# Optimization experiments

Measured on AMD Instinct MI355X. Metric: run time of the kernel, lower is better.

## Reference

```python
import jax, jax.numpy as jnp
import numpy as np

B, H, N_OBS, N_DIR = 4096, 1024, 128, 64
MAX_ITER, LR_ITER, TOL = 10, 1e-3, 1e-3


def _norm(x):
    # row-wise L2 normalization, matching self.norm
    return x / (jnp.linalg.norm(x, axis=1, keepdims=True) + 1e-6)


def setup_inputs() -> dict:
    key = jax.random.key(0)
    ks = jax.random.split(key, 6)
    directions = jax.random.randint(ks[0], (B,), 0, N_DIR)
    obs = jax.random.randint(ks[1], (B,), 0, N_OBS)
    Wr = jax.random.normal(ks[2], (H, H), jnp.float32)
    Win = jax.random.normal(ks[3], (H, N_DIR), jnp.float32)
    Wout = jax.random.normal(ks[4], (N_OBS, H), jnp.float32) * 2.0
    prev_states = _norm(jax.random.normal(ks[5], (B, H), jnp.float32))
    return dict(directions=directions, obs=obs, Wr=Wr, Win=Win,
                Wout=Wout, prev_states=prev_states)


def reference(directions, obs, Wr, Win, Wout, prev_states):
    dtype = Wr.dtype
    dir_e = jax.nn.one_hot(directions, N_DIR, dtype=dtype)  # [B, n_dir]
    obs_e = jax.nn.one_hot(obs, N_OBS, dtype=dtype)         # [B, n_obs]

    drive = jnp.einsum('hd,bd->bh', Win, dir_e)
    cur = _norm(jax.nn.relu(jnp.einsum('hk,bk->bh', Wr, prev_states) + drive))
    prev = prev_states
    done = jnp.array(False)

    def step(carry, _):
        prev, cur, done = carry
        # while condition: |mean(prev - cur)| > tol (checked before each update)
        cond = jnp.abs(jnp.mean(prev - cur)) > TOL
        active = jnp.logical_and(jnp.logical_not(done), cond)

        logits = jnp.einsum('oh,bh->bo', Wout, cur)          # [B, n_obs]
        f = jax.nn.softmax(logits, axis=1)
        eps_p = obs_e - f
        # softmax-Jacobian vector product: J @ v = f * (v - <f, v>)
        Jv = f * (eps_p - jnp.sum(f * eps_p, axis=1, keepdims=True))
        eps_g = cur - jax.nn.relu(jnp.einsum('hk,bk->bh', Wr, prev) + drive)
        new_cur = _norm(cur + LR_ITER * (-eps_g + jnp.einsum('oh,bo->bh', Wout, Jv)))

        prev_n = jnp.where(active, cur, prev)
        cur_n = jnp.where(active, new_cur, cur)
        done_n = jnp.logical_or(done, jnp.logical_not(cond))
        return (prev_n, cur_n, done_n), None

    (prev, cur, done), _ = jax.lax.scan(step, (prev, cur, done), None, length=MAX_ITER)
    next_obs_preds = jax.nn.softmax(jnp.einsum('oh,bh->bo', Wout, cur), axis=1)
    return next_obs_preds, cur
```

## Files before the change

kernel.cpp:

```cpp
#include <hip/hip_runtime.h>
#include <cstdint>
#include <cstddef>

#define B_    4096
#define H_    1024
#define NOBS  128
#define NDIR  64
#define MAXIT 10
#define LRI   1e-3f
#define TOLC  1e-3
#define KS_   8

typedef __bf16 bf16x8 __attribute__((ext_vector_type(8)));
typedef float  f32x4  __attribute__((ext_vector_type(4)));

__device__ __forceinline__ ushort f2bf(float x) {
    uint32_t u = __float_as_uint(x);
    u += 0x7FFFu + ((u >> 16) & 1u);
    return (ushort)(u >> 16);
}
__device__ __forceinline__ float bf2f(ushort h) {
    return __uint_as_float(((uint32_t)h) << 16);
}

template<int ROWS>
__device__ __forceinline__ void stage_tile(ushort* dst, const ushort* src,
                                           size_t rowbase, int ld, int k0,
                                           int tid, int wid)
{
    constexpr int ITERS = ROWS * 4 / 256;
#pragma unroll
    for (int cc = 0; cc < ITERS; ++cc) {
        const int c = cc * 256 + tid;
        const int r = c >> 2, s = c & 3;
        const int ks = ((s ^ ((r >> 1) & 3)) << 3);
        const ushort* g = src + (rowbase + r) * (size_t)ld + k0 + ks;
        __builtin_amdgcn_global_load_lds(
            (const __attribute__((address_space(1))) void*)g,
            (__attribute__((address_space(3))) void*)(dst + (cc * 256 + wid * 64) * 8),
            16, 0, 0);
    }
}

template<int EPI, int BN>
__global__ __launch_bounds__(256)
void gemm_pipe_k(const ushort* __restrict__ Ahi, const ushort* __restrict__ Alo, int lda,
                 const ushort* __restrict__ Bhi, const ushort* __restrict__ Blo, int ldb,
                 float* __restrict__ O,
                 const int* __restrict__ dirs, const float* __restrict__ Win,
                 const float* __restrict__ Cin,
                 const int* gate)
{
    if (gate && *gate == 0) return;

    constexpr int NFR = BN / 32;
    constexpr int NST = (EPI == 0) ? H_ / 32
                      : (EPI == 1) ? (H_ / KS_) / 32
                                   : NOBS / 32;

    __shared__ ushort sA[2][2][128 * 32];
    __shared__ ushort sB[2][2][BN * 32];

    const int tid = threadIdx.x, lane = tid & 63, wid = tid >> 6;
    const size_t m0  = (size_t)blockIdx.y * 128;
    const size_t bn0 = (EPI == 1) ? 0 : (size_t)blockIdx.x * BN;
    const int kbase  = (EPI == 1) ? blockIdx.x * (H_ / KS_) : 0;
    const int wr = wid >> 1, wc = wid & 1;

    f32x4 acc[4][NFR];
#pragma unroll
    for (int i = 0; i < 4; ++i)
#pragma unroll
        for (int j = 0; j < NFR; ++j) acc[i][j] = (f32x4){0.f, 0.f, 0.f, 0.f};

    const int rsel = lane & 15;
    const int kb   = lane >> 4;

    stage_tile<128>(sA[0][0], Ahi, m0, lda, kbase, tid, wid);
    stage_tile<128>(sA[0][1], Alo, m0, lda, kbase, tid, wid);
    stage_tile<BN >(sB[0][0], Bhi, bn0, ldb, kbase, tid, wid);
    stage_tile<BN >(sB[0][1], Blo, bn0, ldb, kbase, tid, wid);
    __syncthreads();

#pragma unroll 2
    for (int t = 0; t < NST; ++t) {
        const int cur = t & 1;
        if (t + 1 < NST) {
            const int k0 = kbase + (t + 1) * 32;
            stage_tile<128>(sA[cur ^ 1][0], Ahi, m0, lda, k0, tid, wid);
            stage_tile<128>(sA[cur ^ 1][1], Alo, m0, lda, k0, tid, wid);
            stage_tile<BN >(sB[cur ^ 1][0], Bhi, bn0, ldb, k0, tid, wid);
            stage_tile<BN >(sB[cur ^ 1][1], Blo, bn0, ldb, k0, tid, wid);
        }

        bf16x8 ah[4], al[4], bh[NFR], bl[NFR];
#pragma unroll
        for (int f = 0; f < 4; ++f) {
            const int arow = wr * 64 + f * 16 + rsel;
            const int aoff = arow * 32 + ((kb ^ ((arow >> 1) & 3)) << 3);
            ah[f] = *(const bf16x8*)&sA[cur][0][aoff];
            al[f] = *(const bf16x8*)&sA[cur][1][aoff];
        }
#pragma unroll
        for (int f = 0; f < NFR; ++f) {
            const int brow = wc * (BN / 2) + f * 16 + rsel;
            const int boff = brow * 32 + ((kb ^ ((brow >> 1) & 3)) << 3);
            bh[f] = *(const bf16x8*)&sB[cur][0][boff];
            bl[f] = *(const bf16x8*)&sB[cur][1][boff];
        }

#pragma unroll
        for (int i = 0; i < 4; ++i)
#pragma unroll
            for (int j = 0; j < NFR; ++j) {
                acc[i][j] = __builtin_amdgcn_mfma_f32_16x16x32_bf16(ah[i], bh[j], acc[i][j], 0, 0, 0);
                acc[i][j] = __builtin_amdgcn_mfma_f32_16x16x32_bf16(ah[i], bl[j], acc[i][j], 0, 0, 0);
                acc[i][j] = __builtin_amdgcn_mfma_f32_16x16x32_bf16(al[i], bh[j], acc[i][j], 0, 0, 0);
            }
        __syncthreads();
    }

    float* pout = (EPI == 1) ? O + (size_t)blockIdx.x * B_ * NOBS : O;
#pragma unroll
    for (int i = 0; i < 4; ++i) {
#pragma unroll
        for (int r = 0; r < 4; ++r) {
            const size_t row = m0 + wr * 64 + i * 16 + (lane >> 4) * 4 + r;
            int dd = 0;
            if (EPI == 0) dd = dirs[row];
#pragma unroll
            for (int j = 0; j < NFR; ++j) {
                const size_t col = bn0 + wc * (BN / 2) + j * 16 + (lane & 15);
                if (EPI == 0) {
                    const float v = acc[i][j][r] + Win[col * NDIR + dd];
                    pout[row * H_ + col] = fmaxf(v, 0.f);
                } else if (EPI == 1) {
                    pout[row * NOBS + col] = acc[i][j][r];
                } else {
                    const size_t idx = row * H_ + col;
                    const float c = Cin[idx], rv = pout[idx];
                    pout[idx] = c + LRI * ((rv - c) + acc[i][j][r]);
                }
            }
        }
    }
}

template<int MODE>
__global__ __launch_bounds__(256)
void softjv_k(const float* __restrict__ part, const int* __restrict__ obs,
              ushort* __restrict__ Jhi, ushort* __restrict__ Jlo,
              float* __restrict__ probs, const int* gate)
{
    if (MODE == 0 && gate && *gate == 0) return;
    const int wid = threadIdx.x >> 6, lane = threadIdx.x & 63;
    const int b = blockIdx.x * 4 + wid;
    float x0 = 0.f, x1 = 0.f;
#pragma unroll
    for (int kb = 0; kb < KS_; ++kb) {
        const float* p = part + ((size_t)kb * B_ + b) * NOBS;
        x0 += p[lane]; x1 += p[lane + 64];
    }
    float mx = fmaxf(x0, x1);
#pragma unroll
    for (int off = 32; off > 0; off >>= 1) mx = fmaxf(mx, __shfl_xor(mx, off, 64));
    const float e0 = expf(x0 - mx), e1 = expf(x1 - mx);
    float s = e0 + e1;
#pragma unroll
    for (int off = 32; off > 0; off >>= 1) s += __shfl_xor(s, off, 64);
    const float f0 = e0 / s, f1 = e1 / s;
    if (MODE == 1) {
        probs[(size_t)b * NOBS + lane]      = f0;
        probs[(size_t)b * NOBS + lane + 64] = f1;
        return;
    }
    const int o = obs[b];
    const float ep0 = ((lane == o) ? 1.f : 0.f) - f0;
    const float ep1 = ((lane + 64 == o) ? 1.f : 0.f) - f1;
    float d = f0 * ep0 + f1 * ep1;
#pragma unroll
    for (int off = 32; off > 0; off >>= 1) d += __shfl_xor(d, off, 64);
    const float j0 = f0 * (ep0 - d), j1 = f1 * (ep1 - d);
    const ushort h0 = f2bf(j0), h1 = f2bf(j1);
    Jhi[(size_t)b * NOBS + lane]      = h0;
    Jlo[(size_t)b * NOBS + lane]      = f2bf(j0 - bf2f(h0));
    Jhi[(size_t)b * NOBS + lane + 64] = h1;
    Jlo[(size_t)b * NOBS + lane + 64] = f2bf(j1 - bf2f(h1));
}

template<bool ADV>
__global__ __launch_bounds__(256)
void normadv_k(const float* __restrict__ T, float* __restrict__ C,
               ushort* __restrict__ Chi, ushort* __restrict__ Clo,
               ushort* __restrict__ Phi, ushort* __restrict__ Plo,
               const float* __restrict__ oldsum, float* __restrict__ rowsum,
               double* __restrict__ rowpart, const int* gate)
{
    if (gate && *gate == 0) return;
    const int b = blockIdx.x, tid = threadIdx.x;
    const size_t ro = (size_t)b * H_;

    if (ADV) {
        ((ushort4*)(Phi + ro))[tid] = ((const ushort4*)(Chi + ro))[tid];
        ((ushort4*)(Plo + ro))[tid] = ((const ushort4*)(Clo + ro))[tid];
    }

    const float4 v = ((const float4*)(T + ro))[tid];
    float ss = v.x * v.x + v.y * v.y + v.z * v.z + v.w * v.w;
    float sm = v.x + v.y + v.z + v.w;
#pragma unroll
    for (int off = 32; off > 0; off >>= 1) {
        ss += __shfl_down(ss, off, 64);
        sm += __shfl_down(sm, off, 64);
    }
    __shared__ float w1[4], w2[4];
    const int lane = tid & 63, wid = tid >> 6;
    if (lane == 0) { w1[wid] = ss; w2[wid] = sm; }
    __syncthreads();
    const float tot = w1[0] + w1[1] + w1[2] + w1[3];
    const float smt = w2[0] + w2[1] + w2[2] + w2[3];
    const float d = sqrtf(tot) + 1e-6f;

    float4 o;
    o.x = v.x / d; o.y = v.y / d; o.z = v.z / d; o.w = v.w / d;
    ((float4*)(C + ro))[tid] = o;
    ushort4 h, l;
    h.x = f2bf(o.x); l.x = f2bf(o.x - bf2f(h.x));
    h.y = f2bf(o.y); l.y = f2bf(o.y - bf2f(h.y));
    h.z = f2bf(o.z); l.z = f2bf(o.z - bf2f(h.z));
    h.w = f2bf(o.w); l.w = f2bf(o.w - bf2f(h.w));
    ((ushort4*)(Chi + ro))[tid] = h;
    ((ushort4*)(Clo + ro))[tid] = l;

    if (tid == 0) {
        const float news = smt / d;
        rowpart[b] = (double)oldsum[b] - (double)news;
        rowsum[b]  = news;
    }
}

__global__ __launch_bounds__(256)
void cond_fin_k(const double* __restrict__ rowpart, int* active, int* done)
{
    if (*done) { if (threadIdx.x == 0) *active = 0; return; }
    __shared__ double wsum[4];
    double s = 0.0;
    for (int i = threadIdx.x; i < B_; i += 256) s += rowpart[i];
#pragma unroll
    for (int off = 32; off > 0; off >>= 1) s += __shfl_down(s, off, 64);
    const int lane = threadIdx.x & 63, wid = threadIdx.x >> 6;
    if (lane == 0) wsum[wid] = s;
    __syncthreads();
    if (threadIdx.x == 0) {
        const double mean = (wsum[0] + wsum[1] + wsum[2] + wsum[3]) / (double)((size_t)B_ * H_);
        const int c = (fabs(mean) > TOLC) ? 1 : 0;
        *active = c;
        if (!c) *done = 1;
    }
}

__global__ __launch_bounds__(256)
void split_k(const float* __restrict__ x, ushort* __restrict__ hi,
             ushort* __restrict__ lo)
{
    const size_t i = (size_t)blockIdx.x * 256 + threadIdx.x;
    const float4 v = ((const float4*)x)[i];
    ushort4 h, l;
    h.x = f2bf(v.x); l.x = f2bf(v.x - bf2f(h.x));
    h.y = f2bf(v.y); l.y = f2bf(v.y - bf2f(h.y));
    h.z = f2bf(v.z); l.z = f2bf(v.z - bf2f(h.z));
    h.w = f2bf(v.w); l.w = f2bf(v.w - bf2f(h.w));
    ((ushort4*)hi)[i] = h;
    ((ushort4*)lo)[i] = l;
}

__global__ __launch_bounds__(256)
void prev0_prep_k(const float* __restrict__ prev0, ushort* __restrict__ Phi,
                  ushort* __restrict__ Plo, float* __restrict__ prevsum0)
{
    const int b = blockIdx.x, tid = threadIdx.x;
    const size_t ro = (size_t)b * H_;
    const float4 v = ((const float4*)(prev0 + ro))[tid];
    ushort4 h, l;
    h.x = f2bf(v.x); l.x = f2bf(v.x - bf2f(h.x));
    h.y = f2bf(v.y); l.y = f2bf(v.y - bf2f(h.y));
    h.z = f2bf(v.z); l.z = f2bf(v.z - bf2f(h.z));
    h.w = f2bf(v.w); l.w = f2bf(v.w - bf2f(h.w));
    ((ushort4*)(Phi + ro))[tid] = h;
    ((ushort4*)(Plo + ro))[tid] = l;
    float sm = v.x + v.y + v.z + v.w;
#pragma unroll
    for (int off = 32; off > 0; off >>= 1) sm += __shfl_down(sm, off, 64);
    __shared__ float w2[4];
    const int lane = tid & 63, wid = tid >> 6;
    if (lane == 0) w2[wid] = sm;
    __syncthreads();
    if (tid == 0) prevsum0[b] = w2[0] + w2[1] + w2[2] + w2[3];
}

__global__ __launch_bounds__(256)
void prep_wout_k(const float* __restrict__ Wout, ushort* __restrict__ Whi,
                 ushort* __restrict__ Wlo, ushort* __restrict__ WThi,
                 ushort* __restrict__ WTlo)
{
    const int idx = blockIdx.x * 256 + threadIdx.x;
    const float w = Wout[idx];
    const ushort h = f2bf(w), l = f2bf(w - bf2f(h));
    Whi[idx] = h; Wlo[idx] = l;
    const int o = idx >> 10, hh = idx & 1023;
    WThi[(size_t)hh * NOBS + o] = h;
    WTlo[(size_t)hh * NOBS + o] = l;
}

__global__ __launch_bounds__(256)
void copy_k(const float* __restrict__ src, float* __restrict__ dst)
{
    const size_t i = (size_t)blockIdx.x * 256 + threadIdx.x;
    ((float4*)dst)[i] = ((const float4*)src)[i];
}

__global__ void flags_init_k(int* flags) { flags[0] = 0; flags[1] = 0; }

extern "C" void kernel_launch(void* const* d_in, const int* in_sizes, int n_in,
                              void* d_out, int out_size, void* d_ws, size_t ws_size,
                              hipStream_t stream)
{
    const int*   dirs  = (const int*)d_in[0];
    const int*   obs   = (const int*)d_in[1];
    const float* Wr    = (const float*)d_in[2];
    const float* Win   = (const float*)d_in[3];
    const float* Wout  = (const float*)d_in[4];
    const float* prev0 = (const float*)d_in[5];
    float* out = (float*)d_out;

    const size_t SZ = (size_t)B_ * H_;
    float*  C    = (float*)d_ws;
    float*  T    = C + SZ;
    float*  part = T + SZ;
    ushort* Chi  = (ushort*)(part + (size_t)KS_ * B_ * NOBS);
    ushort* Clo  = Chi + SZ;
    ushort* Phi  = Clo + SZ;
    ushort* Plo  = Phi + SZ;
    ushort* Wrhi = Plo + SZ;
    ushort* Wrlo = Wrhi + (size_t)H_ * H_;
    ushort* Whi  = Wrlo + (size_t)H_ * H_;
    ushort* Wlo  = Whi + (size_t)NOBS * H_;
    ushort* WThi = Wlo + (size_t)NOBS * H_;
    ushort* WTlo = WThi + (size_t)H_ * NOBS;
    ushort* Jhi  = WTlo + (size_t)H_ * NOBS;
    ushort* Jlo  = Jhi + (size_t)B_ * NOBS;
    double* rowpart = (double*)(Jlo + (size_t)B_ * NOBS);
    float* prevsum0 = (float*)(rowpart + B_);
    float* rowsumC  = prevsum0 + B_;
    int* flags  = (int*)(rowsumC + B_);
    int* done   = flags;
    int* active = flags + 1;

    const dim3 blk(256);
    const dim3 gBig(H_ / 64, B_ / 128);
    const dim3 gLog(KS_, B_ / 128);

    flags_init_k<<<1, 1, 0, stream>>>(flags);
    split_k<<<(H_ * H_ / 4) / 256, blk, 0, stream>>>(Wr, Wrhi, Wrlo);
    prev0_prep_k<<<B_, blk, 0, stream>>>(prev0, Phi, Plo, prevsum0);
    prep_wout_k<<<(NOBS * H_) / 256, blk, 0, stream>>>(Wout, Whi, Wlo, WThi, WTlo);

    gemm_pipe_k<0, 64><<<gBig, blk, 0, stream>>>(
        Phi, Plo, H_, Wrhi, Wrlo, H_, T, dirs, Win, nullptr, nullptr);
    normadv_k<false><<<B_, blk, 0, stream>>>(
        T, C, Chi, Clo, nullptr, nullptr, prevsum0, rowsumC, rowpart, nullptr);

    for (int it = 0; it < MAXIT; ++it) {
        cond_fin_k<<<1, blk, 0, stream>>>(rowpart, active, done);

        if (it > 0)
            gemm_pipe_k<0, 64><<<gBig, blk, 0, stream>>>(
                Phi, Plo, H_, Wrhi, Wrlo, H_, T, dirs, Win, nullptr, active);
        gemm_pipe_k<1, 128><<<gLog, blk, 0, stream>>>(
            Chi, Clo, H_, Whi, Wlo, H_, part, nullptr, nullptr, nullptr, active);
        softjv_k<0><<<B_ / 4, blk, 0, stream>>>(part, obs, Jhi, Jlo, nullptr, active);
        gemm_pipe_k<2, 64><<<gBig, blk, 0, stream>>>(
            Jhi, Jlo, NOBS, WThi, WTlo, NOBS, T, nullptr, nullptr, C, active);
        normadv_k<true><<<B_, blk, 0, stream>>>(
            T, C, Chi, Clo, Phi, Plo, rowsumC, rowsumC, rowpart, active);
    }

    gemm_pipe_k<1, 128><<<gLog, blk, 0, stream>>>(
        Chi, Clo, H_, Whi, Wlo, H_, part, nullptr, nullptr, nullptr, nullptr);
    softjv_k<1><<<B_ / 4, blk, 0, stream>>>(part, obs, nullptr, nullptr, out, nullptr);
    copy_k<<<SZ / 4 / 256, blk, 0, stream>>>(C, out + (size_t)B_ * NOBS);
}
```

Measured before the change: 314.3 us.

## Add dedicated 128x128 Wr GEMM kernel with 32x32 MFMA and triple-buffered loads

Replaces the generic pipelined GEMM used for the dominant Wr @ prev product with a specialized kernel. It uses 128x128 output tiles, 32x32x16 bf16 MFMA instructions and a three-stage LDS ring with explicit vmcnt waits and barriers, so global loads run two tiles ahead. The generic kernel loses its Wr epilogue and fully unrolls its short K loops. The aim is more operand reuse per LDS read and better hiding of load latency. The cost is higher LDS use (96 KB per block), which lowers occupancy, and half as many blocks for this GEMM.

New measurement: 320.5 us. About the same (+2.0%).

```diff
diff --git a/kernel.cpp b/kernel.cpp
--- a/kernel.cpp
+++ b/kernel.cpp
@@ -13,6 +13,7 @@
 
 typedef __bf16 bf16x8 __attribute__((ext_vector_type(8)));
 typedef float  f32x4  __attribute__((ext_vector_type(4)));
+typedef float  f32x16 __attribute__((ext_vector_type(16)));
 
 __device__ __forceinline__ ushort f2bf(float x) {
     uint32_t u = __float_as_uint(x);
@@ -42,21 +43,128 @@
     }
 }
 
+__global__ __launch_bounds__(256)
+void wr_gemm_k(const ushort* __restrict__ Ahi, const ushort* __restrict__ Alo,
+               const ushort* __restrict__ Bhi, const ushort* __restrict__ Blo,
+               float* __restrict__ O,
+               const int* __restrict__ dirs, const float* __restrict__ Win,
+               const int* gate)
+{
+    if (gate && *gate == 0) return;
+
+    constexpr int NST = H_ / 32;
+    __shared__ ushort sA[3][2][128 * 32];
+    __shared__ ushort sB[3][2][128 * 32];
+
+    const int tid = threadIdx.x, lane = tid & 63, wid = tid >> 6;
+    const size_t m0 = (size_t)blockIdx.y * 128;
+    const size_t n0 = (size_t)blockIdx.x * 128;
+    const int wr = wid >> 1, wc = wid & 1;
+
+    f32x16 acc[2][2];
+#pragma unroll
+    for (int i = 0; i < 2; ++i)
+#pragma unroll
+        for (int j = 0; j < 2; ++j)
+#pragma unroll
+            for (int r = 0; r < 16; ++r) acc[i][j][r] = 0.f;
+
+    stage_tile<128>(sA[0][0], Ahi, m0, H_, 0, tid, wid);
+    stage_tile<128>(sA[0][1], Alo, m0, H_, 0, tid, wid);
+    stage_tile<128>(sB[0][0], Bhi, n0, H_, 0, tid, wid);
+    stage_tile<128>(sB[0][1], Blo, n0, H_, 0, tid, wid);
+    __builtin_amdgcn_sched_barrier(0);
+    stage_tile<128>(sA[1][0], Ahi, m0, H_, 32, tid, wid);
+    stage_tile<128>(sA[1][1], Alo, m0, H_, 32, tid, wid);
+    stage_tile<128>(sB[1][0], Bhi, n0, H_, 32, tid, wid);
+    stage_tile<128>(sB[1][1], Blo, n0, H_, 32, tid, wid);
+    __builtin_amdgcn_sched_barrier(0);
+
+    int cur = 0;
+#pragma unroll 1
+    for (int t = 0; t < NST; ++t) {
+        if (t + 1 < NST) asm volatile("s_waitcnt vmcnt(8)" ::: "memory");
+        else             asm volatile("s_waitcnt vmcnt(0)" ::: "memory");
+        __builtin_amdgcn_sched_barrier(0);
+        __builtin_amdgcn_s_barrier();
+        __builtin_amdgcn_sched_barrier(0);
+
+        if (t + 2 < NST) {
+            const int nbuf = (cur >= 1) ? cur - 1 : cur + 2;
+            const int k0 = (t + 2) * 32;
+            stage_tile<128>(sA[nbuf][0], Ahi, m0, H_, k0, tid, wid);
+            stage_tile<128>(sA[nbuf][1], Alo, m0, H_, k0, tid, wid);
+            stage_tile<128>(sB[nbuf][0], Bhi, n0, H_, k0, tid, wid);
+            stage_tile<128>(sB[nbuf][1], Blo, n0, H_, k0, tid, wid);
+        }
+        __builtin_amdgcn_sched_barrier(0);
+
+        const ushort* pAh = sA[cur][0];
+        const ushort* pAl = sA[cur][1];
+        const ushort* pBh = sB[cur][0];
+        const ushort* pBl = sB[cur][1];
+
+#pragma unroll
+        for (int s = 0; s < 2; ++s) {
+            bf16x8 ah[2], al[2], bh[2], bl[2];
+            const int e8 = s * 2 + (lane >> 5);
+#pragma unroll
+            for (int mb = 0; mb < 2; ++mb) {
+                const int row = wr * 64 + mb * 32 + (lane & 31);
+                const int off = row * 32 + ((e8 ^ ((row >> 1) & 3)) << 3);
+                ah[mb] = *(const bf16x8*)&pAh[off];
+                al[mb] = *(const bf16x8*)&pAl[off];
+            }
+#pragma unroll
+            for (int nb = 0; nb < 2; ++nb) {
+                const int row = wc * 64 + nb * 32 + (lane & 31);
+                const int off = row * 32 + ((e8 ^ ((row >> 1) & 3)) << 3);
+                bh[nb] = *(const bf16x8*)&pBh[off];
+                bl[nb] = *(const bf16x8*)&pBl[off];
+            }
+#pragma unroll
+            for (int mb = 0; mb < 2; ++mb)
+#pragma unroll
+                for (int nb = 0; nb < 2; ++nb) {
+                    acc[mb][nb] = __builtin_amdgcn_mfma_f32_32x32x16_bf16(ah[mb], bh[nb], acc[mb][nb], 0, 0, 0);
+                    acc[mb][nb] = __builtin_amdgcn_mfma_f32_32x32x16_bf16(ah[mb], bl[nb], acc[mb][nb], 0, 0, 0);
+                    acc[mb][nb] = __builtin_amdgcn_mfma_f32_32x32x16_bf16(al[mb], bh[nb], acc[mb][nb], 0, 0, 0);
+                }
+        }
+
+        __builtin_amdgcn_sched_barrier(0);
+        __builtin_amdgcn_s_barrier();
+        cur = (cur == 2) ? 0 : cur + 1;
+    }
+
+#pragma unroll
+    for (int mb = 0; mb < 2; ++mb)
+#pragma unroll
+        for (int reg = 0; reg < 16; ++reg) {
+            const size_t row = m0 + wr * 64 + mb * 32 +
+                               (reg & 3) + 8 * (reg >> 2) + 4 * (lane >> 5);
+            const int dd = dirs[row];
+#pragma unroll
+            for (int nb = 0; nb < 2; ++nb) {
+                const size_t col = n0 + wc * 64 + nb * 32 + (lane & 31);
+                const float v = acc[mb][nb][reg] + Win[col * NDIR + dd];
+                O[row * H_ + col] = fmaxf(v, 0.f);
+            }
+        }
+}
+
 template<int EPI, int BN>
 __global__ __launch_bounds__(256)
 void gemm_pipe_k(const ushort* __restrict__ Ahi, const ushort* __restrict__ Alo, int lda,
                  const ushort* __restrict__ Bhi, const ushort* __restrict__ Blo, int ldb,
                  float* __restrict__ O,
-                 const int* __restrict__ dirs, const float* __restrict__ Win,
                  const float* __restrict__ Cin,
                  const int* gate)
 {
     if (gate && *gate == 0) return;
 
     constexpr int NFR = BN / 32;
-    constexpr int NST = (EPI == 0) ? H_ / 32
-                      : (EPI == 1) ? (H_ / KS_) / 32
-                                   : NOBS / 32;
+    constexpr int NST = (EPI == 1) ? (H_ / KS_) / 32 : NOBS / 32;
 
     __shared__ ushort sA[2][2][128 * 32];
     __shared__ ushort sB[2][2][BN * 32];
@@ -82,7 +190,7 @@
     stage_tile<BN >(sB[0][1], Blo, bn0, ldb, kbase, tid, wid);
     __syncthreads();
 
-#pragma unroll 2
+#pragma unroll
     for (int t = 0; t < NST; ++t) {
         const int cur = t & 1;
         if (t + 1 < NST) {
@@ -126,15 +234,10 @@
 #pragma unroll
         for (int r = 0; r < 4; ++r) {
             const size_t row = m0 + wr * 64 + i * 16 + (lane >> 4) * 4 + r;
-            int dd = 0;
-            if (EPI == 0) dd = dirs[row];
 #pragma unroll
             for (int j = 0; j < NFR; ++j) {
                 const size_t col = bn0 + wc * (BN / 2) + j * 16 + (lane & 15);
-                if (EPI == 0) {
-                    const float v = acc[i][j][r] + Win[col * NDIR + dd];
-                    pout[row * H_ + col] = fmaxf(v, 0.f);
-                } else if (EPI == 1) {
+                if (EPI == 1) {
                     pout[row * NOBS + col] = acc[i][j][r];
                 } else {
                     const size_t idx = row * H_ + col;
@@ -357,7 +460,8 @@
     int* active = flags + 1;
 
     const dim3 blk(256);
-    const dim3 gBig(H_ / 64, B_ / 128);
+    const dim3 gBig(H_ / 128, B_ / 128);
+    const dim3 gUpd(H_ / 64, B_ / 128);
     const dim3 gLog(KS_, B_ / 128);
 
     flags_init_k<<<1, 1, 0, stream>>>(flags);
@@ -365,8 +469,7 @@
     prev0_prep_k<<<B_, blk, 0, stream>>>(prev0, Phi, Plo, prevsum0);
     prep_wout_k<<<(NOBS * H_) / 256, blk, 0, stream>>>(Wout, Whi, Wlo, WThi, WTlo);
 
-    gemm_pipe_k<0, 64><<<gBig, blk, 0, stream>>>(
-        Phi, Plo, H_, Wrhi, Wrlo, H_, T, dirs, Win, nullptr, nullptr);
+    wr_gemm_k<<<gBig, blk, 0, stream>>>(Phi, Plo, Wrhi, Wrlo, T, dirs, Win, nullptr);
     normadv_k<false><<<B_, blk, 0, stream>>>(
         T, C, Chi, Clo, nullptr, nullptr, prevsum0, rowsumC, rowpart, nullptr);
 
@@ -374,19 +477,18 @@
         cond_fin_k<<<1, blk, 0, stream>>>(rowpart, active, done);
 
         if (it > 0)
-            gemm_pipe_k<0, 64><<<gBig, blk, 0, stream>>>(
-                Phi, Plo, H_, Wrhi, Wrlo, H_, T, dirs, Win, nullptr, active);
+            wr_gemm_k<<<gBig, blk, 0, stream>>>(Phi, Plo, Wrhi, Wrlo, T, dirs, Win, active);
         gemm_pipe_k<1, 128><<<gLog, blk, 0, stream>>>(
-            Chi, Clo, H_, Whi, Wlo, H_, part, nullptr, nullptr, nullptr, active);
+            Chi, Clo, H_, Whi, Wlo, H_, part, nullptr, active);
         softjv_k<0><<<B_ / 4, blk, 0, stream>>>(part, obs, Jhi, Jlo, nullptr, active);
-        gemm_pipe_k<2, 64><<<gBig, blk, 0, stream>>>(
-            Jhi, Jlo, NOBS, WThi, WTlo, NOBS, T, nullptr, nullptr, C, active);
+        gemm_pipe_k<2, 64><<<gUpd, blk, 0, stream>>>(
+            Jhi, Jlo, NOBS, WThi, WTlo, NOBS, T, C, active);
         normadv_k<true><<<B_, blk, 0, stream>>>(
             T, C, Chi, Clo, Phi, Plo, rowsumC, rowsumC, rowpart, active);
     }
 
     gemm_pipe_k<1, 128><<<gLog, blk, 0, stream>>>(
-        Chi, Clo, H_, Whi, Wlo, H_, part, nullptr, nullptr, nullptr, nullptr);
+        Chi, Clo, H_, Whi, Wlo, H_, part, nullptr, nullptr);
     softjv_k<1><<<B_ / 4, blk, 0, stream>>>(part, obs, nullptr, nullptr, out, nullptr);
     copy_k<<<SZ / 4 / 256, blk, 0, stream>>>(C, out + (size_t)B_ * NOBS);
 }
```

## Switch GEMMs from split-bf16 triple MFMA to single fp16 MFMA, fold convergence check into atomics

Applied to the files above, without the earlier changes.

Replaces the hi/lo bf16 split (three MFMAs per tile plus two operand copies) with a single fp16 operand and one f16 MFMA per tile. This halves operand traffic and cuts matrix work by about three times. The block tile shrinks from 128 to 64 rows, doubling the grid. The separate convergence-reduction kernel is removed: each row's residual is added atomically into a per-iteration double slot, and every kernel checks all slots up to the current iteration. The cost is lower precision, since fp16 has a 10-bit mantissa against the roughly 16 bits of the split-bf16 scheme, and Wr values drawn from a normal distribution are cast directly to fp16.

New measurement: 338.7 us. 1.08x slower.

```diff
diff --git a/kernel.cpp b/kernel.cpp
--- a/kernel.cpp
+++ b/kernel.cpp
@@ -11,16 +11,20 @@
 #define TOLC  1e-3
 #define KS_   8
 
-typedef __bf16 bf16x8 __attribute__((ext_vector_type(8)));
-typedef float  f32x4  __attribute__((ext_vector_type(4)));
-
-__device__ __forceinline__ ushort f2bf(float x) {
-    uint32_t u = __float_as_uint(x);
-    u += 0x7FFFu + ((u >> 16) & 1u);
-    return (ushort)(u >> 16);
-}
-__device__ __forceinline__ float bf2f(ushort h) {
-    return __uint_as_float(((uint32_t)h) << 16);
+typedef _Float16 f16x8 __attribute__((ext_vector_type(8)));
+typedef float    f32x4 __attribute__((ext_vector_type(4)));
+
+static __device__ __forceinline__ ushort f2h(float x) {
+    _Float16 h = (_Float16)x;
+    return __builtin_bit_cast(ushort, h);
+}
+
+static __device__ __forceinline__ bool gate_on(const double* slots, int it) {
+    if (it < 0) return true;
+    const double GTH = 1e-3 * (double)B_ * (double)H_;
+    for (int j = 0; j <= it; ++j)
+        if (fabs(slots[j]) <= GTH) return false;
+    return true;
 }
 
 template<int ROWS>
@@ -44,102 +48,94 @@
 
 template<int EPI, int BN>
 __global__ __launch_bounds__(256)
-void gemm_pipe_k(const ushort* __restrict__ Ahi, const ushort* __restrict__ Alo, int lda,
-                 const ushort* __restrict__ Bhi, const ushort* __restrict__ Blo, int ldb,
-                 float* __restrict__ O,
-                 const int* __restrict__ dirs, const float* __restrict__ Win,
-                 const float* __restrict__ Cin,
-                 const int* gate)
-{
-    if (gate && *gate == 0) return;
-
-    constexpr int NFR = BN / 32;
+void gemm_f16_k(const ushort* __restrict__ A, int lda,
+                const ushort* __restrict__ Bt, int ldb,
+                float* __restrict__ O,
+                const int* __restrict__ dirs, const float* __restrict__ Win,
+                const float* __restrict__ Cin,
+                const double* __restrict__ slots, int it)
+{
+    if (!gate_on(slots, it)) return;
+
+    constexpr int FN  = BN / 32;
     constexpr int NST = (EPI == 0) ? H_ / 32
                       : (EPI == 1) ? (H_ / KS_) / 32
                                    : NOBS / 32;
 
-    __shared__ ushort sA[2][2][128 * 32];
-    __shared__ ushort sB[2][2][BN * 32];
+    __shared__ ushort sA[2][64 * 32];
+    __shared__ ushort sB[2][BN * 32];
 
     const int tid = threadIdx.x, lane = tid & 63, wid = tid >> 6;
-    const size_t m0  = (size_t)blockIdx.y * 128;
+    const size_t m0  = (size_t)blockIdx.y * 64;
     const size_t bn0 = (EPI == 1) ? 0 : (size_t)blockIdx.x * BN;
     const int kbase  = (EPI == 1) ? blockIdx.x * (H_ / KS_) : 0;
     const int wr = wid >> 1, wc = wid & 1;
 
-    f32x4 acc[4][NFR];
-#pragma unroll
-    for (int i = 0; i < 4; ++i)
-#pragma unroll
-        for (int j = 0; j < NFR; ++j) acc[i][j] = (f32x4){0.f, 0.f, 0.f, 0.f};
+    f32x4 acc[2][FN];
+#pragma unroll
+    for (int i = 0; i < 2; ++i)
+#pragma unroll
+        for (int j = 0; j < FN; ++j) acc[i][j] = (f32x4){0.f, 0.f, 0.f, 0.f};
 
     const int rsel = lane & 15;
     const int kb   = lane >> 4;
 
-    stage_tile<128>(sA[0][0], Ahi, m0, lda, kbase, tid, wid);
-    stage_tile<128>(sA[0][1], Alo, m0, lda, kbase, tid, wid);
-    stage_tile<BN >(sB[0][0], Bhi, bn0, ldb, kbase, tid, wid);
-    stage_tile<BN >(sB[0][1], Blo, bn0, ldb, kbase, tid, wid);
+    stage_tile<64>(sA[0], A, m0, lda, kbase, tid, wid);
+    stage_tile<BN>(sB[0], Bt, bn0, ldb, kbase, tid, wid);
     __syncthreads();
 
-#pragma unroll 2
+#pragma unroll
     for (int t = 0; t < NST; ++t) {
         const int cur = t & 1;
         if (t + 1 < NST) {
             const int k0 = kbase + (t + 1) * 32;
-            stage_tile<128>(sA[cur ^ 1][0], Ahi, m0, lda, k0, tid, wid);
-            stage_tile<128>(sA[cur ^ 1][1], Alo, m0, lda, k0, tid, wid);
-            stage_tile<BN >(sB[cur ^ 1][0], Bhi, bn0, ldb, k0, tid, wid);
-            stage_tile<BN >(sB[cur ^ 1][1], Blo, bn0, ldb, k0, tid, wid);
+            stage_tile<64>(sA[cur ^ 1], A, m0, lda, k0, tid, wid);
+            stage_tile<BN>(sB[cur ^ 1], Bt, bn0, ldb, k0, tid, wid);
         }
 
-        bf16x8 ah[4], al[4], bh[NFR], bl[NFR];
-#pragma unroll
-        for (int f = 0; f < 4; ++f) {
-            const int arow = wr * 64 + f * 16 + rsel;
+        f16x8 a[2], b[FN];
+#pragma unroll
+        for (int fi = 0; fi < 2; ++fi) {
+            const int arow = wr * 32 + fi * 16 + rsel;
             const int aoff = arow * 32 + ((kb ^ ((arow >> 1) & 3)) << 3);
-            ah[f] = *(const bf16x8*)&sA[cur][0][aoff];
-            al[f] = *(const bf16x8*)&sA[cur][1][aoff];
+            a[fi] = *(const f16x8*)&sA[cur][aoff];
         }
 #pragma unroll
-        for (int f = 0; f < NFR; ++f) {
-            const int brow = wc * (BN / 2) + f * 16 + rsel;
+        for (int fj = 0; fj < FN; ++fj) {
+            const int brow = wc * (BN / 2) + fj * 16 + rsel;
             const int boff = brow * 32 + ((kb ^ ((brow >> 1) & 3)) << 3);
-            bh[f] = *(const bf16x8*)&sB[cur][0][boff];
-            bl[f] = *(const bf16x8*)&sB[cur][1][boff];
+            b[fj] = *(const f16x8*)&sB[cur][boff];
         }
 
 #pragma unroll
-        for (int i = 0; i < 4; ++i)
-#pragma unroll
-            for (int j = 0; j < NFR; ++j) {
-                acc[i][j] = __builtin_amdgcn_mfma_f32_16x16x32_bf16(ah[i], bh[j], acc[i][j], 0, 0, 0);
-                acc[i][j] = __builtin_amdgcn_mfma_f32_16x16x32_bf16(ah[i], bl[j], acc[i][j], 0, 0, 0);
-                acc[i][j] = __builtin_amdgcn_mfma_f32_16x16x32_bf16(al[i], bh[j], acc[i][j], 0, 0, 0);
-            }
+        for (int fi = 0; fi < 2; ++fi)
+#pragma unroll
+            for (int fj = 0; fj < FN; ++fj)
+                acc[fi][fj] = __builtin_amdgcn_mfma_f32_16x16x32_f16(
+                    a[fi], b[fj], acc[fi][fj], 0, 0, 0);
         __syncthreads();
     }
 
     float* pout = (EPI == 1) ? O + (size_t)blockIdx.x * B_ * NOBS : O;
 #pragma unroll
-    for (int i = 0; i < 4; ++i) {
+    for (int fi = 0; fi < 2; ++fi) {
 #pragma unroll
         for (int r = 0; r < 4; ++r) {
-            const size_t row = m0 + wr * 64 + i * 16 + (lane >> 4) * 4 + r;
+            const size_t row = m0 + wr * 32 + fi * 16 + (lane >> 4) * 4 + r;
             int dd = 0;
             if (EPI == 0) dd = dirs[row];
 #pragma unroll
-            for (int j = 0; j < NFR; ++j) {
-                const size_t col = bn0 + wc * (BN / 2) + j * 16 + (lane & 15);
+            for (int fj = 0; fj < FN; ++fj) {
+                const size_t col = bn0 + wc * (BN / 2) + fj * 16 + (lane & 15);
                 if (EPI == 0) {
-                    const float v = acc[i][j][r] + Win[col * NDIR + dd];
+                    const float v = acc[fi][fj][r] + Win[col * NDIR + dd];
                     pout[row * H_ + col] = fmaxf(v, 0.f);
                 } else if (EPI == 1) {
-                    pout[row * NOBS + col] = acc[i][j][r];
+                    pout[row * NOBS + col] = acc[fi][fj][r];
                 } else {
                     const size_t idx = row * H_ + col;
                     const float c = Cin[idx], rv = pout[idx];
-                    pout[idx] = c + LRI * ((rv - c) + acc[i][j][r]);
+                    pout[idx] = c + LRI * ((rv - c) + acc[fi][fj][r]);
                 }
             }
         }
@@ -149,10 +145,10 @@
 template<int MODE>
 __global__ __launch_bounds__(256)
 void softjv_k(const float* __restrict__ part, const int* __restrict__ obs,
-              ushort* __restrict__ Jhi, ushort* __restrict__ Jlo,
-              float* __restrict__ probs, const int* gate)
-{
-    if (MODE == 0 && gate && *gate == 0) return;
+              ushort* __restrict__ Jh, float* __restrict__ probs,
+              const double* __restrict__ slots, int it)
+{
+    if (MODE == 0 && !gate_on(slots, it)) return;
     const int wid = threadIdx.x >> 6, lane = threadIdx.x & 63;
     const int b = blockIdx.x * 4 + wid;
     float x0 = 0.f, x1 = 0.f;
@@ -180,30 +176,24 @@
     float d = f0 * ep0 + f1 * ep1;
 #pragma unroll
     for (int off = 32; off > 0; off >>= 1) d += __shfl_xor(d, off, 64);
-    const float j0 = f0 * (ep0 - d), j1 = f1 * (ep1 - d);
-    const ushort h0 = f2bf(j0), h1 = f2bf(j1);
-    Jhi[(size_t)b * NOBS + lane]      = h0;
-    Jlo[(size_t)b * NOBS + lane]      = f2bf(j0 - bf2f(h0));
-    Jhi[(size_t)b * NOBS + lane + 64] = h1;
-    Jlo[(size_t)b * NOBS + lane + 64] = f2bf(j1 - bf2f(h1));
+    Jh[(size_t)b * NOBS + lane]      = f2h(f0 * (ep0 - d));
+    Jh[(size_t)b * NOBS + lane + 64] = f2h(f1 * (ep1 - d));
 }
 
 template<bool ADV>
 __global__ __launch_bounds__(256)
 void normadv_k(const float* __restrict__ T, float* __restrict__ C,
-               ushort* __restrict__ Chi, ushort* __restrict__ Clo,
-               ushort* __restrict__ Phi, ushort* __restrict__ Plo,
+               ushort* __restrict__ C_h, ushort* __restrict__ P_h,
                const float* __restrict__ oldsum, float* __restrict__ rowsum,
-               double* __restrict__ rowpart, const int* gate)
-{
-    if (gate && *gate == 0) return;
+               double* __restrict__ slotdst,
+               const double* __restrict__ slots, int it)
+{
+    if (!gate_on(slots, it)) return;
     const int b = blockIdx.x, tid = threadIdx.x;
     const size_t ro = (size_t)b * H_;
 
-    if (ADV) {
-        ((ushort4*)(Phi + ro))[tid] = ((const ushort4*)(Chi + ro))[tid];
-        ((ushort4*)(Plo + ro))[tid] = ((const ushort4*)(Clo + ro))[tid];
-    }
+    if (ADV)
+        ((ushort4*)(P_h + ro))[tid] = ((const ushort4*)(C_h + ro))[tid];
 
     const float4 v = ((const float4*)(T + ro))[tid];
     float ss = v.x * v.x + v.y * v.y + v.z * v.z + v.w * v.w;
@@ -224,70 +214,28 @@
     float4 o;
     o.x = v.x / d; o.y = v.y / d; o.z = v.z / d; o.w = v.w / d;
     ((float4*)(C + ro))[tid] = o;
-    ushort4 h, l;
-    h.x = f2bf(o.x); l.x = f2bf(o.x - bf2f(h.x));
-    h.y = f2bf(o.y); l.y = f2bf(o.y - bf2f(h.y));
-    h.z = f2bf(o.z); l.z = f2bf(o.z - bf2f(h.z));
-    h.w = f2bf(o.w); l.w = f2bf(o.w - bf2f(h.w));
-    ((ushort4*)(Chi + ro))[tid] = h;
-    ((ushort4*)(Clo + ro))[tid] = l;
+    ushort4 h;
+    h.x = f2h(o.x); h.y = f2h(o.y); h.z = f2h(o.z); h.w = f2h(o.w);
+    ((ushort4*)(C_h + ro))[tid] = h;
 
     if (tid == 0) {
         const float news = smt / d;
-        rowpart[b] = (double)oldsum[b] - (double)news;
-        rowsum[b]  = news;
-    }
-}
-
-__global__ __launch_bounds__(256)
-void cond_fin_k(const double* __restrict__ rowpart, int* active, int* done)
-{
-    if (*done) { if (threadIdx.x == 0) *active = 0; return; }
-    __shared__ double wsum[4];
-    double s = 0.0;
-    for (int i = threadIdx.x; i < B_; i += 256) s += rowpart[i];
-#pragma unroll
-    for (int off = 32; off > 0; off >>= 1) s += __shfl_down(s, off, 64);
-    const int lane = threadIdx.x & 63, wid = threadIdx.x >> 6;
-    if (lane == 0) wsum[wid] = s;
-    __syncthreads();
-    if (threadIdx.x == 0) {
-        const double mean = (wsum[0] + wsum[1] + wsum[2] + wsum[3]) / (double)((size_t)B_ * H_);
-        const int c = (fabs(mean) > TOLC) ? 1 : 0;
-        *active = c;
-        if (!c) *done = 1;
-    }
-}
-
-__global__ __launch_bounds__(256)
-void split_k(const float* __restrict__ x, ushort* __restrict__ hi,
-             ushort* __restrict__ lo)
-{
-    const size_t i = (size_t)blockIdx.x * 256 + threadIdx.x;
-    const float4 v = ((const float4*)x)[i];
-    ushort4 h, l;
-    h.x = f2bf(v.x); l.x = f2bf(v.x - bf2f(h.x));
-    h.y = f2bf(v.y); l.y = f2bf(v.y - bf2f(h.y));
-    h.z = f2bf(v.z); l.z = f2bf(v.z - bf2f(h.z));
-    h.w = f2bf(v.w); l.w = f2bf(v.w - bf2f(h.w));
-    ((ushort4*)hi)[i] = h;
-    ((ushort4*)lo)[i] = l;
-}
-
-__global__ __launch_bounds__(256)
-void prev0_prep_k(const float* __restrict__ prev0, ushort* __restrict__ Phi,
-                  ushort* __restrict__ Plo, float* __restrict__ prevsum0)
+        atomicAdd(slotdst, (double)oldsum[b] - (double)news);
+        rowsum[b] = news;
+    }
+}
+
+__global__ __launch_bounds__(256)
+void prev0_prep_k(const float* __restrict__ prev0, ushort* __restrict__ P_h,
+                  float* __restrict__ prevsum0, double* __restrict__ slots)
 {
     const int b = blockIdx.x, tid = threadIdx.x;
+    if (b == 0 && tid < 16) slots[tid] = 0.0;
     const size_t ro = (size_t)b * H_;
     const float4 v = ((const float4*)(prev0 + ro))[tid];
-    ushort4 h, l;
-    h.x = f2bf(v.x); l.x = f2bf(v.x - bf2f(h.x));
-    h.y = f2bf(v.y); l.y = f2bf(v.y - bf2f(h.y));
-    h.z = f2bf(v.z); l.z = f2bf(v.z - bf2f(h.z));
-    h.w = f2bf(v.w); l.w = f2bf(v.w - bf2f(h.w));
-    ((ushort4*)(Phi + ro))[tid] = h;
-    ((ushort4*)(Plo + ro))[tid] = l;
+    ushort4 h;
+    h.x = f2h(v.x); h.y = f2h(v.y); h.z = f2h(v.z); h.w = f2h(v.w);
+    ((ushort4*)(P_h + ro))[tid] = h;
     float sm = v.x + v.y + v.z + v.w;
 #pragma unroll
     for (int off = 32; off > 0; off >>= 1) sm += __shfl_down(sm, off, 64);
@@ -299,17 +247,24 @@
 }
 
 __global__ __launch_bounds__(256)
-void prep_wout_k(const float* __restrict__ Wout, ushort* __restrict__ Whi,
-                 ushort* __restrict__ Wlo, ushort* __restrict__ WThi,
-                 ushort* __restrict__ WTlo)
-{
-    const int idx = blockIdx.x * 256 + threadIdx.x;
-    const float w = Wout[idx];
-    const ushort h = f2bf(w), l = f2bf(w - bf2f(h));
-    Whi[idx] = h; Wlo[idx] = l;
-    const int o = idx >> 10, hh = idx & 1023;
-    WThi[(size_t)hh * NOBS + o] = h;
-    WTlo[(size_t)hh * NOBS + o] = l;
+void conv_w_k(const float* __restrict__ Wr, ushort* __restrict__ Wr_h,
+              const float* __restrict__ Wout, ushort* __restrict__ W_h,
+              ushort* __restrict__ WT_h)
+{
+    const int bid = blockIdx.x;
+    if (bid < 1024) {
+        const size_t i = (size_t)bid * 256 + threadIdx.x;
+        const float4 v = ((const float4*)Wr)[i];
+        ushort4 h;
+        h.x = f2h(v.x); h.y = f2h(v.y); h.z = f2h(v.z); h.w = f2h(v.w);
+        ((ushort4*)Wr_h)[i] = h;
+    } else {
+        const int idx = (bid - 1024) * 256 + threadIdx.x;
+        const ushort h = f2h(Wout[idx]);
+        W_h[idx] = h;
+        const int o = idx >> 10, hh = idx & 1023;
+        WT_h[(size_t)hh * NOBS + o] = h;
+    }
 }
 
 __global__ __launch_bounds__(256)
@@ -318,8 +273,6 @@
     const size_t i = (size_t)blockIdx.x * 256 + threadIdx.x;
     ((float4*)dst)[i] = ((const float4*)src)[i];
 }
-
-__global__ void flags_init_k(int* flags) { flags[0] = 0; flags[1] = 0; }
 
 extern "C" void kernel_launch(void* const* d_in, const int* in_sizes, int n_in,
                               void* d_out, int out_size, void* d_ws, size_t ws_size,
@@ -334,59 +287,46 @@
     float* out = (float*)d_out;
 
     const size_t SZ = (size_t)B_ * H_;
-    float*  C    = (float*)d_ws;
-    float*  T    = C + SZ;
-    float*  part = T + SZ;
-    ushort* Chi  = (ushort*)(part + (size_t)KS_ * B_ * NOBS);
-    ushort* Clo  = Chi + SZ;
-    ushort* Phi  = Clo + SZ;
-    ushort* Plo  = Phi + SZ;
-    ushort* Wrhi = Plo + SZ;
-    ushort* Wrlo = Wrhi + (size_t)H_ * H_;
-    ushort* Whi  = Wrlo + (size_t)H_ * H_;
-    ushort* Wlo  = Whi + (size_t)NOBS * H_;
-    ushort* WThi = Wlo + (size_t)NOBS * H_;
-    ushort* WTlo = WThi + (size_t)H_ * NOBS;
-    ushort* Jhi  = WTlo + (size_t)H_ * NOBS;
-    ushort* Jlo  = Jhi + (size_t)B_ * NOBS;
-    double* rowpart = (double*)(Jlo + (size_t)B_ * NOBS);
-    float* prevsum0 = (float*)(rowpart + B_);
-    float* rowsumC  = prevsum0 + B_;
-    int* flags  = (int*)(rowsumC + B_);
-    int* done   = flags;
-    int* active = flags + 1;
+    double* slots    = (double*)d_ws;
+    float*  C        = (float*)(slots + 16);
+    float*  T        = C + SZ;
+    float*  part     = T + SZ;
+    float*  prevsum0 = part + (size_t)KS_ * B_ * NOBS;
+    float*  rowsum   = prevsum0 + B_;
+    ushort* Wr_h     = (ushort*)(rowsum + B_);
+    ushort* W_h      = Wr_h + (size_t)H_ * H_;
+    ushort* WT_h     = W_h + (size_t)NOBS * H_;
+    ushort* C_h      = WT_h + (size_t)H_ * NOBS;
+    ushort* P_h      = C_h + SZ;
+    ushort* J_h      = P_h + SZ;
 
     const dim3 blk(256);
-    const dim3 gBig(H_ / 64, B_ / 128);
-    const dim3 gLog(KS_, B_ / 128);
-
-    flags_init_k<<<1, 1, 0, stream>>>(flags);
-    split_k<<<(H_ * H_ / 4) / 256, blk, 0, stream>>>(Wr, Wrhi, Wrlo);
-    prev0_prep_k<<<B_, blk, 0, stream>>>(prev0, Phi, Plo, prevsum0);
-    prep_wout_k<<<(NOBS * H_) / 256, blk, 0, stream>>>(Wout, Whi, Wlo, WThi, WTlo);
-
-    gemm_pipe_k<0, 64><<<gBig, blk, 0, stream>>>(
-        Phi, Plo, H_, Wrhi, Wrlo, H_, T, dirs, Win, nullptr, nullptr);
+    const dim3 gBig(H_ / 64, B_ / 64);
+    const dim3 gLog(KS_, B_ / 64);
+
+    prev0_prep_k<<<B_, blk, 0, stream>>>(prev0, P_h, prevsum0, slots);
+    conv_w_k<<<1024 + 512, blk, 0, stream>>>(Wr, Wr_h, Wout, W_h, WT_h);
+
+    gemm_f16_k<0, 64><<<gBig, blk, 0, stream>>>(
+        P_h, H_, Wr_h, H_, T, dirs, Win, nullptr, slots, -1);
     normadv_k<false><<<B_, blk, 0, stream>>>(
-        T, C, Chi, Clo, nullptr, nullptr, prevsum0, rowsumC, rowpart, nullptr);
+        T, C, C_h, nullptr, prevsum0, rowsum, slots + 0, slots, -1);
 
     for (int it = 0; it < MAXIT; ++it) {
-        cond_fin_k<<<1, blk, 0, stream>>>(rowpart, active, done);
-
         if (it > 0)
-            gemm_pipe_k<0, 64><<<gBig, blk, 0, stream>>>(
-                Phi, Plo, H_, Wrhi, Wrlo, H_, T, dirs, Win, nullptr, active);
-        gemm_pipe_k<1, 128><<<gLog, blk, 0, stream>>>(
-            Chi, Clo, H_, Whi, Wlo, H_, part, nullptr, nullptr, nullptr, active);
-        softjv_k<0><<<B_ / 4, blk, 0, stream>>>(part, obs, Jhi, Jlo, nullptr, active);
-        gemm_pipe_k<2, 64><<<gBig, blk, 0, stream>>>(
-            Jhi, Jlo, NOBS, WThi, WTlo, NOBS, T, nullptr, nullptr, C, active);
+            gemm_f16_k<0, 64><<<gBig, blk, 0, stream>>>(
+                P_h, H_, Wr_h, H_, T, dirs, Win, nullptr, slots, it);
+        gemm_f16_k<1, 128><<<gLog, blk, 0, stream>>>(
+            C_h, H_, W_h, H_, part, nullptr, nullptr, nullptr, slots, it);
+        softjv_k<0><<<B_ / 4, blk, 0, stream>>>(part, obs, J_h, nullptr, slots, it);
+        gemm_f16_k<2, 64><<<gBig, blk, 0, stream>>>(
+            J_h, NOBS, WT_h, NOBS, T, nullptr, nullptr, C, slots, it);
         normadv_k<true><<<B_, blk, 0, stream>>>(
-            T, C, Chi, Clo, Phi, Plo, rowsumC, rowsumC, rowpart, active);
-    }
-
-    gemm_pipe_k<1, 128><<<gLog, blk, 0, stream>>>(
-        Chi, Clo, H_, Whi, Wlo, H_, part, nullptr, nullptr, nullptr, nullptr);
-    softjv_k<1><<<B_ / 4, blk, 0, stream>>>(part, obs, nullptr, nullptr, out, nullptr);
+            T, C, C_h, P_h, rowsum, rowsum, slots + it + 1, slots, it);
+    }
+
+    gemm_f16_k<1, 128><<<gLog, blk, 0, stream>>>(
+        C_h, H_, W_h, H_, part, nullptr, nullptr, nullptr, slots, -1);
+    softjv_k<1><<<B_ / 4, blk, 0, stream>>>(part, obs, nullptr, out, slots, -1);
     copy_k<<<SZ / 4 / 256, blk, 0, stream>>>(C, out + (size_t)B_ * NOBS);
 }
```
